# Kernel tuning notes

Hardware: AMD Instinct MI355X
Metric: run time of the kernel (lower is better)

## Reference

```python
import jax, jax.numpy as jnp
import numpy as np

N_QUBITS = 14
W_MUL = (2.0 ** 0.5) * (5.0 ** -0.5)  # he_std = gain * 5**-0.5, lrmul = 1
TWO_PI = 2.0 * np.pi


def _rx(t):
    c = jnp.cos(t / 2); s = jnp.sin(t / 2)
    return jnp.stack([jnp.stack([c + 0j, -1j * s]), jnp.stack([-1j * s, c + 0j])])


def _ry(t):
    c = jnp.cos(t / 2); s = jnp.sin(t / 2)
    return jnp.stack([jnp.stack([c + 0j, -s + 0j]), jnp.stack([s + 0j, c + 0j])])


def _rz(t):
    e = jnp.exp(-0.5j * t); z = jnp.zeros_like(e)
    return jnp.stack([jnp.stack([e, z]), jnp.stack([z, jnp.conj(e)])])


def _apply_1q(state, gate, q):
    # state: (B,) + (2,)*n ; apply 2x2 gate on qubit q (axis q+1)
    ax = q + 1
    out = jnp.tensordot(gate, state, axes=([1], [ax]))  # new qubit axis at front
    return jnp.moveaxis(out, 0, ax)


_CNOT = jnp.array([[1, 0, 0, 0],
                   [0, 1, 0, 0],
                   [0, 0, 0, 1],
                   [0, 0, 1, 0]], dtype=jnp.complex64).reshape(2, 2, 2, 2)


def _apply_cnot(state, c, t):
    # _CNOT indices: [out_c, out_t, in_c, in_t]
    out = jnp.tensordot(_CNOT, state, axes=([2, 3], [c + 1, t + 1]))
    return jnp.moveaxis(out, (0, 1), (c + 1, t + 1))


def _rot_layer(state, params, gates):
    # per-qubit triple of rotations: params[3*i + j] for gate j on qubit i
    for i in range(N_QUBITS):
        for j, g in enumerate(gates):
            state = _apply_1q(state, g(params[3 * i + j]), i)
    return state


def _ring_of_cnot(state):
    for i in range(N_QUBITS):
        state = _apply_cnot(state, i, (i + 1) % N_QUBITS)
    return state


def _forward(x_real, x_imag, weight):
    n = N_QUBITS
    B = x_real.shape[0]
    psi = (x_real + 1j * x_imag).astype(jnp.complex64).reshape((B,) + (2,) * n)
    w = weight * W_MUL
    layers = [(_rx, _ry, _rz),  # XYZLayer
              (_ry, _rz, _ry),  # YZYLayer
              (_rz, _ry, _rx),  # ZYXLayer
              (_rx, _rz, _rx),  # XZXLayer
              (_ry, _rz, _ry)]  # YZYLayer
    for li, gates in enumerate(layers):
        psi = _rot_layer(psi, w[3 * n * li: 3 * n * (li + 1)], gates)
        if li < len(layers) - 1:
            psi = _ring_of_cnot(psi)
    Z = jnp.array([[1, 0], [0, -1]], dtype=jnp.complex64)
    zpsi = _apply_1q(psi, Z, 0)
    # <psi| Z_0 |psi> (original: conj(psi) row-vector @ (Z_0 psi) column-vector, take real)
    ev = jnp.sum(jnp.conj(psi) * zpsi, axis=tuple(range(1, n + 1))).real
    return ev.reshape(B, 1)  # matches torch (B,1,1).squeeze(-1)


def setup_inputs() -> dict:
    key = jax.random.key(0)
    k1, k2, k3 = jax.random.split(key, 3)
    B = 512
    dim = 2 ** N_QUBITS
    x_real = jax.random.normal(k1, (B, 1, dim), dtype=jnp.float32)
    x_imag = jax.random.normal(k2, (B, 1, dim), dtype=jnp.float32)
    weight = jax.random.uniform(k3, (15 * N_QUBITS,), dtype=jnp.float32) * TWO_PI
    return {"x_real": x_real, "x_imag": x_imag, "weight": weight}


def reference(x_real, x_imag, weight):
    return _forward(x_real, x_imag, weight)
```

## Files before the change

### kernel.cpp

```cpp
#include <hip/hip_runtime.h>
#include <hip/hip_bf16.h>

#define NQ   14
#define DIM  16384
#define BLK  1024
#define WMUL 0.6324555320336759f

typedef float v2f __attribute__((ext_vector_type(2)));

struct C2 { float x, y; };
__device__ inline C2 cmulc(C2 a, C2 b){ return C2{a.x*b.x - a.y*b.y, a.x*b.y + a.y*b.x}; }
__device__ inline C2 caddc(C2 a, C2 b){ return C2{a.x+b.x, a.y+b.y}; }
__device__ inline void mm2(const C2* a, const C2* b, C2* o) {
    o[0] = caddc(cmulc(a[0],b[0]), cmulc(a[1],b[2]));
    o[1] = caddc(cmulc(a[0],b[1]), cmulc(a[1],b[3]));
    o[2] = caddc(cmulc(a[2],b[0]), cmulc(a[3],b[2]));
    o[3] = caddc(cmulc(a[2],b[1]), cmulc(a[3],b[3]));
}
__device__ inline void build_gate(int ty, float t, C2* g) {
    float sn, cs;
    __sincosf(0.5f * t, &sn, &cs);
    if (ty == 0) {
        g[0] = C2{cs, 0.f}; g[1] = C2{0.f, -sn};
        g[2] = C2{0.f, -sn}; g[3] = C2{cs, 0.f};
    } else if (ty == 1) {
        g[0] = C2{cs, 0.f}; g[1] = C2{-sn, 0.f};
        g[2] = C2{sn, 0.f}; g[3] = C2{cs, 0.f};
    } else {
        g[0] = C2{cs, -sn}; g[1] = C2{0.f, 0.f};
        g[2] = C2{0.f, 0.f}; g[3] = C2{cs, sn};
    }
}
__device__ const int TYPES[5][3] = {
    {0,1,2},
    {1,2,1},
    {2,1,0},
    {0,2,0},
    {1,2,1},
};

__device__ inline constexpr uint32_t slotf(uint32_t i){
    return i ^ (((i>>4) ^ (i>>8) ^ (i>>12)) & 15u);
}
template<int B> __device__ inline uint32_t ins0(uint32_t t){
    return ((t & ~((1u<<B)-1u)) << 1) | (t & ((1u<<B)-1u));
}
template<int B0,int B1,int B2> __device__ inline uint32_t expand3(uint32_t t){
    return ins0<B2>(ins0<B1>(ins0<B0>(t)));
}
template<int B0,int B1,int B2> __device__ inline constexpr uint32_t rmask3(int r){
    return ((r&1)?(1u<<B0):0u) | ((r&2)?(1u<<B1):0u) | ((r&4)?(1u<<B2):0u);
}

template<int J>
__device__ inline void rot8(v2f* v, const v2f* __restrict__ g){
    const v2f a00=g[0], b00=g[1], a01=g[2], b01=g[3];
    const v2f a10=g[4], b10=g[5], a11=g[6], b11=g[7];
    #pragma unroll
    for (int r = 0; r < 8; ++r){
        if (!(r & (1 << J))) {
            v2f x0 = v[r], x1 = v[r | (1 << J)];
            v2f s0 = x0.yx, s1 = x1.yx;
            v2f y0 = a00*x0 + b00*s0 + a01*x1 + b01*s1;
            v2f y1 = a10*x0 + b10*s0 + a11*x1 + b11*s1;
            v[r] = y0; v[r | (1<<J)] = y1;
        }
    }
}
template<int C, int T>
__device__ inline void cnot8(v2f* v){
    #pragma unroll
    for (int r = 0; r < 8; ++r){
        if ((r & (1 << C)) && !(r & (1 << T))) {
            v2f tt = v[r]; v[r] = v[r | (1 << T)]; v[r | (1 << T)] = tt;
        }
    }
}

__global__ __launch_bounds__(BLK) void qsim_kernel(
        const float* __restrict__ xr, const float* __restrict__ xi,
        const float* __restrict__ w, float* __restrict__ out) {
    __shared__ v2f s[DIM];
    __shared__ v2f gmp[5 * NQ * 8];
    __shared__ float red[BLK / 64];

    const int b   = blockIdx.x;
    const uint32_t tid = threadIdx.x;

    if (tid < 5 * NQ) {
        const int li = tid / NQ, q = tid % NQ;
        C2 M[4], G[4], T[4];
        #pragma unroll
        for (int j = 0; j < 3; ++j) {
            float t = w[3 * NQ * li + 3 * q + j] * WMUL;
            build_gate(TYPES[li][j], t, G);
            if (j == 0) { M[0]=G[0]; M[1]=G[1]; M[2]=G[2]; M[3]=G[3]; }
            else { mm2(G, M, T); M[0]=T[0]; M[1]=T[1]; M[2]=T[2]; M[3]=T[3]; }
        }
        #pragma unroll
        for (int k = 0; k < 4; ++k) {
            gmp[tid * 8 + k * 2 + 0] = v2f{ M[k].x, M[k].x};
            gmp[tid * 8 + k * 2 + 1] = v2f{-M[k].y, M[k].y};
        }
    }
    __syncthreads();

    const float* xrb = xr + (size_t)b * DIM;
    const float* xib = xi + (size_t)b * DIM;

    #define GMP(li, q) (&gmp[((li) * NQ + (q)) * 8])

    #define PASS(B0, B1, B2, ...)                                                  \
        _Pragma("unroll 1")                                                        \
        for (uint32_t sl = 0; sl < 2; ++sl) {                                      \
            const uint32_t t  = tid + sl * BLK;                                    \
            const uint32_t sb = slotf(expand3<B0,B1,B2>(t));                       \
            v2f v[8];                                                              \
            _Pragma("unroll")                                                      \
            for (int r = 0; r < 8; ++r)                                            \
                v[r] = s[sb ^ slotf(rmask3<B0,B1,B2>(r))];                         \
            __VA_ARGS__                                                            \
            _Pragma("unroll")                                                      \
            for (int r = 0; r < 8; ++r)                                            \
                s[sb ^ slotf(rmask3<B0,B1,B2>(r))] = v[r];                         \
        }                                                                          \
        __syncthreads();

    #pragma unroll 1
    for (int li = 0; li < 3; ++li) {
        #pragma unroll 1
        for (uint32_t sl = 0; sl < 2; ++sl) {
            const uint32_t t = tid + sl * BLK;
            v2f v[8];
            if (li == 0) {
                #pragma unroll
                for (int r = 0; r < 8; ++r) {
                    uint32_t i = t | ((uint32_t)r << 11);
                    v[r] = v2f{xrb[i], xib[i]};
                }
            } else {
                const uint32_t sb = slotf(expand3<11,12,13>(t));
                #pragma unroll
                for (int r = 0; r < 8; ++r)
                    v[r] = s[sb ^ slotf(rmask3<11,12,13>(r))];
            }
            rot8<2>(v, GMP(li,0)); rot8<1>(v, GMP(li,1)); rot8<0>(v, GMP(li,2));
            cnot8<2,1>(v); cnot8<1,0>(v);
            const uint32_t sb = slotf(expand3<11,12,13>(t));
            #pragma unroll
            for (int r = 0; r < 8; ++r)
                s[sb ^ slotf(rmask3<11,12,13>(r))] = v[r];
        }
        __syncthreads();

        PASS(9,10,11, rot8<1>(v, GMP(li,3));  rot8<0>(v, GMP(li,4));  cnot8<2,1>(v); cnot8<1,0>(v);)
        PASS(7,8,9,   rot8<1>(v, GMP(li,5));  rot8<0>(v, GMP(li,6));  cnot8<2,1>(v); cnot8<1,0>(v);)
        PASS(5,6,7,   rot8<1>(v, GMP(li,7));  rot8<0>(v, GMP(li,8));  cnot8<2,1>(v); cnot8<1,0>(v);)
        PASS(3,4,5,   rot8<1>(v, GMP(li,9));  rot8<0>(v, GMP(li,10)); cnot8<2,1>(v); cnot8<1,0>(v);)
        PASS(1,2,3,   rot8<1>(v, GMP(li,11)); rot8<0>(v, GMP(li,12)); cnot8<2,1>(v); cnot8<1,0>(v);)
        PASS(0,1,13,  rot8<0>(v, GMP(li,13)); cnot8<1,0>(v); cnot8<0,2>(v);)
    }

    PASS(11,12,13, rot8<2>(v, GMP(3,0));  rot8<1>(v, GMP(3,1));  rot8<0>(v, GMP(3,2));
                   cnot8<2,1>(v); cnot8<1,0>(v);
                   rot8<1>(v, GMP(4,1));)
    PASS(9,10,11,  rot8<1>(v, GMP(3,3));  rot8<0>(v, GMP(3,4));
                   cnot8<2,1>(v); cnot8<1,0>(v);
                   rot8<2>(v, GMP(4,2));  rot8<1>(v, GMP(4,3));)
    PASS(7,8,9,    rot8<1>(v, GMP(3,5));  rot8<0>(v, GMP(3,6));
                   cnot8<2,1>(v); cnot8<1,0>(v);
                   rot8<2>(v, GMP(4,4));  rot8<1>(v, GMP(4,5));)
    PASS(5,6,7,    rot8<1>(v, GMP(3,7));  rot8<0>(v, GMP(3,8));
                   cnot8<2,1>(v); cnot8<1,0>(v);
                   rot8<2>(v, GMP(4,6));  rot8<1>(v, GMP(4,7));)
    PASS(3,4,5,    rot8<1>(v, GMP(3,9));  rot8<0>(v, GMP(3,10));
                   cnot8<2,1>(v); cnot8<1,0>(v);
                   rot8<2>(v, GMP(4,8));  rot8<1>(v, GMP(4,9));)
    PASS(1,2,3,    rot8<1>(v, GMP(3,11)); rot8<0>(v, GMP(3,12));
                   cnot8<2,1>(v); cnot8<1,0>(v);
                   rot8<2>(v, GMP(4,10)); rot8<1>(v, GMP(4,11));)

    float local = 0.f;
    #pragma unroll 1
    for (uint32_t sl = 0; sl < 2; ++sl) {
        const uint32_t t  = tid + sl * BLK;
        const uint32_t sb = slotf(expand3<0,1,13>(t));
        v2f v[8];
        #pragma unroll
        for (int r = 0; r < 8; ++r)
            v[r] = s[sb ^ slotf(rmask3<0,1,13>(r))];
        rot8<0>(v, GMP(3,13));
        cnot8<1,0>(v); cnot8<0,2>(v);
        rot8<1>(v, GMP(4,12)); rot8<0>(v, GMP(4,13)); rot8<2>(v, GMP(4,0));
        #pragma unroll
        for (int r = 0; r < 8; ++r) {
            v2f p = v[r] * v[r];
            float m = p.x + p.y;
            local += (r & 4) ? -m : m;
        }
    }

    #pragma unroll
    for (int off = 32; off > 0; off >>= 1) local += __shfl_down(local, off);
    const int lane = tid & 63, wid = tid >> 6;
    if (lane == 0) red[wid] = local;
    __syncthreads();
    if (tid == 0) {
        float t = 0.f;
        #pragma unroll
        for (int k = 0; k < BLK / 64; ++k) t += red[k];
        out[b] = t;
    }
}

extern "C" void kernel_launch(void* const* d_in, const int* in_sizes, int n_in,
                              void* d_out, int out_size, void* d_ws, size_t ws_size,
                              hipStream_t stream) {
    const float* xr = (const float*)d_in[0];
    const float* xi = (const float*)d_in[1];
    const float* w  = (const float*)d_in[2];
    float* out = (float*)d_out;
    const int B = out_size;
    qsim_kernel<<<B, BLK, 0, stream>>>(xr, xi, w, out);
}
```

Baseline: 130.0 us.

## Process four qubits per shared-memory pass with 16 amplitudes per thread

Each thread now holds 16 amplitudes (4 qubit axes) in registers instead of 8 over two slots. Each pass therefore covers three new qubits, which cuts the number of shared-memory sweeps and __syncthreads barriers per layer. The cost is higher register pressure at a 1024-thread block, which could cause spills or lower occupancy.

Result: slower. 180.9 us (+39.2%).

```diff
diff --git a/kernel.cpp b/kernel.cpp
--- a/kernel.cpp
+++ b/kernel.cpp
@@ -45,19 +45,20 @@
 template<int B> __device__ inline uint32_t ins0(uint32_t t){
     return ((t & ~((1u<<B)-1u)) << 1) | (t & ((1u<<B)-1u));
 }
-template<int B0,int B1,int B2> __device__ inline uint32_t expand3(uint32_t t){
-    return ins0<B2>(ins0<B1>(ins0<B0>(t)));
-}
-template<int B0,int B1,int B2> __device__ inline constexpr uint32_t rmask3(int r){
-    return ((r&1)?(1u<<B0):0u) | ((r&2)?(1u<<B1):0u) | ((r&4)?(1u<<B2):0u);
+template<int B0,int B1,int B2,int B3> __device__ inline uint32_t expand4(uint32_t t){
+    return ins0<B3>(ins0<B2>(ins0<B1>(ins0<B0>(t))));
+}
+template<int B0,int B1,int B2,int B3> __device__ inline constexpr uint32_t rmask4(int r){
+    return ((r&1)?(1u<<B0):0u) | ((r&2)?(1u<<B1):0u)
+         | ((r&4)?(1u<<B2):0u) | ((r&8)?(1u<<B3):0u);
 }
 
 template<int J>
-__device__ inline void rot8(v2f* v, const v2f* __restrict__ g){
+__device__ inline void rot16(v2f* v, const v2f* __restrict__ g){
     const v2f a00=g[0], b00=g[1], a01=g[2], b01=g[3];
     const v2f a10=g[4], b10=g[5], a11=g[6], b11=g[7];
     #pragma unroll
-    for (int r = 0; r < 8; ++r){
+    for (int r = 0; r < 16; ++r){
         if (!(r & (1 << J))) {
             v2f x0 = v[r], x1 = v[r | (1 << J)];
             v2f s0 = x0.yx, s1 = x1.yx;
@@ -68,9 +69,9 @@
     }
 }
 template<int C, int T>
-__device__ inline void cnot8(v2f* v){
+__device__ inline void cnot16(v2f* v){
     #pragma unroll
-    for (int r = 0; r < 8; ++r){
+    for (int r = 0; r < 16; ++r){
         if ((r & (1 << C)) && !(r & (1 << T))) {
             v2f tt = v[r]; v[r] = v[r | (1 << T)]; v[r | (1 << T)] = tt;
         }
@@ -110,93 +111,84 @@
 
     #define GMP(li, q) (&gmp[((li) * NQ + (q)) * 8])
 
-    #define PASS(B0, B1, B2, ...)                                                  \
-        _Pragma("unroll 1")                                                        \
-        for (uint32_t sl = 0; sl < 2; ++sl) {                                      \
-            const uint32_t t  = tid + sl * BLK;                                    \
-            const uint32_t sb = slotf(expand3<B0,B1,B2>(t));                       \
-            v2f v[8];                                                              \
+    #define PASS(B0, B1, B2, B3, ...)                                              \
+        {                                                                          \
+            const uint32_t sb = slotf(expand4<B0,B1,B2,B3>(tid));                  \
+            v2f v[16];                                                             \
             _Pragma("unroll")                                                      \
-            for (int r = 0; r < 8; ++r)                                            \
-                v[r] = s[sb ^ slotf(rmask3<B0,B1,B2>(r))];                         \
+            for (int r = 0; r < 16; ++r)                                           \
+                v[r] = s[sb ^ slotf(rmask4<B0,B1,B2,B3>(r))];                      \
             __VA_ARGS__                                                            \
             _Pragma("unroll")                                                      \
-            for (int r = 0; r < 8; ++r)                                            \
-                s[sb ^ slotf(rmask3<B0,B1,B2>(r))] = v[r];                         \
+            for (int r = 0; r < 16; ++r)                                           \
+                s[sb ^ slotf(rmask4<B0,B1,B2,B3>(r))] = v[r];                      \
         }                                                                          \
         __syncthreads();
 
     #pragma unroll 1
     for (int li = 0; li < 3; ++li) {
-        #pragma unroll 1
-        for (uint32_t sl = 0; sl < 2; ++sl) {
-            const uint32_t t = tid + sl * BLK;
-            v2f v[8];
+        {
+            v2f v[16];
             if (li == 0) {
                 #pragma unroll
-                for (int r = 0; r < 8; ++r) {
-                    uint32_t i = t | ((uint32_t)r << 11);
+                for (int r = 0; r < 16; ++r) {
+                    uint32_t i = tid | ((uint32_t)r << 10);
                     v[r] = v2f{xrb[i], xib[i]};
                 }
             } else {
-                const uint32_t sb = slotf(expand3<11,12,13>(t));
+                const uint32_t sb = slotf(expand4<10,11,12,13>(tid));
                 #pragma unroll
-                for (int r = 0; r < 8; ++r)
-                    v[r] = s[sb ^ slotf(rmask3<11,12,13>(r))];
+                for (int r = 0; r < 16; ++r)
+                    v[r] = s[sb ^ slotf(rmask4<10,11,12,13>(r))];
             }
-            rot8<2>(v, GMP(li,0)); rot8<1>(v, GMP(li,1)); rot8<0>(v, GMP(li,2));
-            cnot8<2,1>(v); cnot8<1,0>(v);
-            const uint32_t sb = slotf(expand3<11,12,13>(t));
+            rot16<3>(v, GMP(li,0)); rot16<2>(v, GMP(li,1));
+            rot16<1>(v, GMP(li,2)); rot16<0>(v, GMP(li,3));
+            cnot16<3,2>(v); cnot16<2,1>(v); cnot16<1,0>(v);
+            const uint32_t sb = slotf(expand4<10,11,12,13>(tid));
             #pragma unroll
-            for (int r = 0; r < 8; ++r)
-                s[sb ^ slotf(rmask3<11,12,13>(r))] = v[r];
+            for (int r = 0; r < 16; ++r)
+                s[sb ^ slotf(rmask4<10,11,12,13>(r))] = v[r];
         }
         __syncthreads();
 
-        PASS(9,10,11, rot8<1>(v, GMP(li,3));  rot8<0>(v, GMP(li,4));  cnot8<2,1>(v); cnot8<1,0>(v);)
-        PASS(7,8,9,   rot8<1>(v, GMP(li,5));  rot8<0>(v, GMP(li,6));  cnot8<2,1>(v); cnot8<1,0>(v);)
-        PASS(5,6,7,   rot8<1>(v, GMP(li,7));  rot8<0>(v, GMP(li,8));  cnot8<2,1>(v); cnot8<1,0>(v);)
-        PASS(3,4,5,   rot8<1>(v, GMP(li,9));  rot8<0>(v, GMP(li,10)); cnot8<2,1>(v); cnot8<1,0>(v);)
-        PASS(1,2,3,   rot8<1>(v, GMP(li,11)); rot8<0>(v, GMP(li,12)); cnot8<2,1>(v); cnot8<1,0>(v);)
-        PASS(0,1,13,  rot8<0>(v, GMP(li,13)); cnot8<1,0>(v); cnot8<0,2>(v);)
-    }
-
-    PASS(11,12,13, rot8<2>(v, GMP(3,0));  rot8<1>(v, GMP(3,1));  rot8<0>(v, GMP(3,2));
-                   cnot8<2,1>(v); cnot8<1,0>(v);
-                   rot8<1>(v, GMP(4,1));)
-    PASS(9,10,11,  rot8<1>(v, GMP(3,3));  rot8<0>(v, GMP(3,4));
-                   cnot8<2,1>(v); cnot8<1,0>(v);
-                   rot8<2>(v, GMP(4,2));  rot8<1>(v, GMP(4,3));)
-    PASS(7,8,9,    rot8<1>(v, GMP(3,5));  rot8<0>(v, GMP(3,6));
-                   cnot8<2,1>(v); cnot8<1,0>(v);
-                   rot8<2>(v, GMP(4,4));  rot8<1>(v, GMP(4,5));)
-    PASS(5,6,7,    rot8<1>(v, GMP(3,7));  rot8<0>(v, GMP(3,8));
-                   cnot8<2,1>(v); cnot8<1,0>(v);
-                   rot8<2>(v, GMP(4,6));  rot8<1>(v, GMP(4,7));)
-    PASS(3,4,5,    rot8<1>(v, GMP(3,9));  rot8<0>(v, GMP(3,10));
-                   cnot8<2,1>(v); cnot8<1,0>(v);
-                   rot8<2>(v, GMP(4,8));  rot8<1>(v, GMP(4,9));)
-    PASS(1,2,3,    rot8<1>(v, GMP(3,11)); rot8<0>(v, GMP(3,12));
-                   cnot8<2,1>(v); cnot8<1,0>(v);
-                   rot8<2>(v, GMP(4,10)); rot8<1>(v, GMP(4,11));)
+        PASS(7,8,9,10, rot16<2>(v, GMP(li,4)); rot16<1>(v, GMP(li,5)); rot16<0>(v, GMP(li,6));
+                       cnot16<3,2>(v); cnot16<2,1>(v); cnot16<1,0>(v);)
+        PASS(4,5,6,7,  rot16<2>(v, GMP(li,7)); rot16<1>(v, GMP(li,8)); rot16<0>(v, GMP(li,9));
+                       cnot16<3,2>(v); cnot16<2,1>(v); cnot16<1,0>(v);)
+        PASS(1,2,3,4,  rot16<2>(v, GMP(li,10)); rot16<1>(v, GMP(li,11)); rot16<0>(v, GMP(li,12));
+                       cnot16<3,2>(v); cnot16<2,1>(v); cnot16<1,0>(v);)
+        PASS(0,1,2,13, rot16<0>(v, GMP(li,13)); cnot16<1,0>(v); cnot16<0,3>(v);)
+    }
+
+    PASS(10,11,12,13, rot16<3>(v, GMP(3,0));  rot16<2>(v, GMP(3,1));
+                      rot16<1>(v, GMP(3,2));  rot16<0>(v, GMP(3,3));
+                      cnot16<3,2>(v); cnot16<2,1>(v); cnot16<1,0>(v);
+                      rot16<2>(v, GMP(4,1));  rot16<1>(v, GMP(4,2));)
+    PASS(7,8,9,10,    rot16<2>(v, GMP(3,4));  rot16<1>(v, GMP(3,5));  rot16<0>(v, GMP(3,6));
+                      cnot16<3,2>(v); cnot16<2,1>(v); cnot16<1,0>(v);
+                      rot16<3>(v, GMP(4,3));  rot16<2>(v, GMP(4,4));  rot16<1>(v, GMP(4,5));)
+    PASS(4,5,6,7,     rot16<2>(v, GMP(3,7));  rot16<1>(v, GMP(3,8));  rot16<0>(v, GMP(3,9));
+                      cnot16<3,2>(v); cnot16<2,1>(v); cnot16<1,0>(v);
+                      rot16<3>(v, GMP(4,6));  rot16<2>(v, GMP(4,7));  rot16<1>(v, GMP(4,8));)
+    PASS(1,2,3,4,     rot16<2>(v, GMP(3,10)); rot16<1>(v, GMP(3,11)); rot16<0>(v, GMP(3,12));
+                      cnot16<3,2>(v); cnot16<2,1>(v); cnot16<1,0>(v);
+                      rot16<3>(v, GMP(4,9));  rot16<2>(v, GMP(4,10)); rot16<1>(v, GMP(4,11));)
 
     float local = 0.f;
-    #pragma unroll 1
-    for (uint32_t sl = 0; sl < 2; ++sl) {
-        const uint32_t t  = tid + sl * BLK;
-        const uint32_t sb = slotf(expand3<0,1,13>(t));
-        v2f v[8];
-        #pragma unroll
-        for (int r = 0; r < 8; ++r)
-            v[r] = s[sb ^ slotf(rmask3<0,1,13>(r))];
-        rot8<0>(v, GMP(3,13));
-        cnot8<1,0>(v); cnot8<0,2>(v);
-        rot8<1>(v, GMP(4,12)); rot8<0>(v, GMP(4,13)); rot8<2>(v, GMP(4,0));
-        #pragma unroll
-        for (int r = 0; r < 8; ++r) {
+    {
+        const uint32_t sb = slotf(expand4<0,1,2,13>(tid));
+        v2f v[16];
+        #pragma unroll
+        for (int r = 0; r < 16; ++r)
+            v[r] = s[sb ^ slotf(rmask4<0,1,2,13>(r))];
+        rot16<0>(v, GMP(3,13));
+        cnot16<1,0>(v); cnot16<0,3>(v);
+        rot16<1>(v, GMP(4,12)); rot16<0>(v, GMP(4,13)); rot16<3>(v, GMP(4,0));
+        #pragma unroll
+        for (int r = 0; r < 16; ++r) {
             v2f p = v[r] * v[r];
             float m = p.x + p.y;
-            local += (r & 4) ? -m : m;
+            local += (r & 8) ? -m : m;
         }
     }
 
```

## Map qubits onto wavefront lanes and use cross-lane swizzles to cut shared-memory passes

Applied to the files above, without the earlier changes.

Restructures the state-vector simulation so each thread holds 3 qubits in registers while 6 more qubits map onto wavefront lane bits. Rotations and CNOTs on lane qubits use ds_swizzle and shfl_xor exchanges. This cuts the number of LDS round-trip passes and barriers from about 25 to 9 and uses a new swizzle for bank-conflict avoidance. The trade-off is extra cross-lane shuffle instructions per gate and intricate qubit-to-index bookkeeping that risks correctness errors.

New measurement: 217.8 us. +67.6%, slower.

```diff
diff --git a/kernel.cpp b/kernel.cpp
--- a/kernel.cpp
+++ b/kernel.cpp
@@ -1,5 +1,4 @@
 #include <hip/hip_runtime.h>
-#include <hip/hip_bf16.h>
 
 #define NQ   14
 #define DIM  16384
@@ -39,21 +38,24 @@
     {1,2,1},
 };
 
-__device__ inline constexpr uint32_t slotf(uint32_t i){
-    return i ^ (((i>>4) ^ (i>>8) ^ (i>>12)) & 15u);
-}
-template<int B> __device__ inline uint32_t ins0(uint32_t t){
-    return ((t & ~((1u<<B)-1u)) << 1) | (t & ((1u<<B)-1u));
-}
-template<int B0,int B1,int B2> __device__ inline uint32_t expand3(uint32_t t){
-    return ins0<B2>(ins0<B1>(ins0<B0>(t)));
-}
-template<int B0,int B1,int B2> __device__ inline constexpr uint32_t rmask3(int r){
-    return ((r&1)?(1u<<B0):0u) | ((r&2)?(1u<<B1):0u) | ((r&4)?(1u<<B2):0u);
+__device__ __forceinline__ constexpr uint32_t slotf2(uint32_t i){
+    return i ^ ((((i>>4) ^ (i>>8) ^ ((i>>12)<<2)) & 15u));
+}
+
+template<int M>
+__device__ __forceinline__ v2f shflx(v2f x){
+    if constexpr (M < 32) {
+        constexpr int pat = 0x1F | (M << 10);
+        int a = __builtin_amdgcn_ds_swizzle(__float_as_int(x.x), pat);
+        int b = __builtin_amdgcn_ds_swizzle(__float_as_int(x.y), pat);
+        return v2f{__int_as_float(a), __int_as_float(b)};
+    } else {
+        return v2f{__shfl_xor(x.x, 32, 64), __shfl_xor(x.y, 32, 64)};
+    }
 }
 
 template<int J>
-__device__ inline void rot8(v2f* v, const v2f* __restrict__ g){
+__device__ __forceinline__ void rot8(v2f* v, const v2f* __restrict__ g){
     const v2f a00=g[0], b00=g[1], a01=g[2], b01=g[3];
     const v2f a10=g[4], b10=g[5], a11=g[6], b11=g[7];
     #pragma unroll
@@ -67,15 +69,46 @@
         }
     }
 }
+
+template<int LM>
+__device__ __forceinline__ void rotL(v2f* v, const v2f* __restrict__ g, uint32_t lane){
+    const bool hi = (lane & LM) != 0;
+    const v2f c1 = hi ? g[6] : g[0];
+    const v2f c2 = hi ? g[7] : g[1];
+    const v2f c3 = hi ? g[4] : g[2];
+    const v2f c4 = hi ? g[5] : g[3];
+    #pragma unroll
+    for (int r = 0; r < 8; ++r){
+        v2f x  = v[r];
+        v2f xp = shflx<LM>(x);
+        v[r] = c1*x + c2*x.yx + c3*xp + c4*xp.yx;
+    }
+}
+
 template<int C, int T>
-__device__ inline void cnot8(v2f* v){
+__device__ __forceinline__ void cnotRR(v2f* v){
+    #pragma unroll
+    for (int r = 0; r < 8; ++r)
+        if ((r & (1<<C)) && !(r & (1<<T))) {
+            v2f t = v[r]; v[r] = v[r|(1<<T)]; v[r|(1<<T)] = t;
+        }
+}
+template<int C, int TM>
+__device__ __forceinline__ void cnotRL(v2f* v){
+    #pragma unroll
+    for (int r = 0; r < 8; ++r)
+        if (r & (1<<C)) v[r] = shflx<TM>(v[r]);
+}
+template<int CM, int TM>
+__device__ __forceinline__ void cnotLL(v2f* v, uint32_t lane){
+    const bool c = (lane & CM) != 0;
     #pragma unroll
     for (int r = 0; r < 8; ++r){
-        if ((r & (1 << C)) && !(r & (1 << T))) {
-            v2f tt = v[r]; v[r] = v[r | (1 << T)]; v[r | (1 << T)] = tt;
-        }
-    }
-}
+        v2f p = shflx<TM>(v[r]);
+        v[r] = c ? p : v[r];
+    }
+}
+
 
 __global__ __launch_bounds__(BLK) void qsim_kernel(
         const float* __restrict__ xr, const float* __restrict__ xi,
@@ -85,7 +118,8 @@
     __shared__ float red[BLK / 64];
 
     const int b   = blockIdx.x;
-    const uint32_t tid = threadIdx.x;
+    const uint32_t tid  = threadIdx.x;
+    const uint32_t lane = tid & 63u;
 
     if (tid < 5 * NQ) {
         const int li = tid / NQ, q = tid % NQ;
@@ -110,100 +144,107 @@
 
     #define GMP(li, q) (&gmp[((li) * NQ + (q)) * 8])
 
-    #define PASS(B0, B1, B2, ...)                                                  \
-        _Pragma("unroll 1")                                                        \
-        for (uint32_t sl = 0; sl < 2; ++sl) {                                      \
-            const uint32_t t  = tid + sl * BLK;                                    \
-            const uint32_t sb = slotf(expand3<B0,B1,B2>(t));                       \
-            v2f v[8];                                                              \
-            _Pragma("unroll")                                                      \
-            for (int r = 0; r < 8; ++r)                                            \
-                v[r] = s[sb ^ slotf(rmask3<B0,B1,B2>(r))];                         \
-            __VA_ARGS__                                                            \
-            _Pragma("unroll")                                                      \
-            for (int r = 0; r < 8; ++r)                                            \
-                s[sb ^ slotf(rmask3<B0,B1,B2>(r))] = v[r];                         \
-        }                                                                          \
+    #pragma unroll 1
+    for (uint32_t sl = 0; sl < 2; ++sl) {
+        const uint32_t t = tid + sl * BLK;
+        v2f v[8];
+        #pragma unroll
+        for (int r = 0; r < 8; ++r) {
+            uint32_t i = t | ((uint32_t)r << 11);
+            v[r] = v2f{xrb[i], xib[i]};
+        }
+        rot8<2>(v, GMP(0,0)); rot8<1>(v, GMP(0,1)); rot8<0>(v, GMP(0,2));
+        rotL<1 >(v, GMP(0,13), lane); rotL<2 >(v, GMP(0,12), lane);
+        rotL<4 >(v, GMP(0,11), lane); rotL<8 >(v, GMP(0,10), lane);
+        rotL<16>(v, GMP(0,9),  lane); rotL<32>(v, GMP(0,8),  lane);
+        cnotRR<2,1>(v);
+        cnotRR<1,0>(v);
+        const uint32_t sb = slotf2(t);
+        #pragma unroll
+        for (int r = 0; r < 8; ++r) s[sb ^ slotf2((uint32_t)r << 11)] = v[r];
+    }
+    __syncthreads();
+
+    #define PASS_M(...)                                                         \
+        _Pragma("unroll 1")                                                     \
+        for (uint32_t sl = 0; sl < 2; ++sl) {                                   \
+            const uint32_t base = (lane << 3) | ((tid >> 6) & 7u)               \
+                                | (((tid >> 9) & 1u) << 12) | (sl << 13);       \
+            const uint32_t sb = slotf2(base);                                   \
+            v2f v[8];                                                           \
+            _Pragma("unroll")                                                   \
+            for (int r = 0; r < 8; ++r) v[r] = s[sb ^ slotf2((uint32_t)r<<9)];  \
+            __VA_ARGS__                                                         \
+            _Pragma("unroll")                                                   \
+            for (int r = 0; r < 8; ++r) s[sb ^ slotf2((uint32_t)r<<9)] = v[r];  \
+        }                                                                       \
         __syncthreads();
 
-    #pragma unroll 1
-    for (int li = 0; li < 3; ++li) {
-        #pragma unroll 1
-        for (uint32_t sl = 0; sl < 2; ++sl) {
-            const uint32_t t = tid + sl * BLK;
-            v2f v[8];
-            if (li == 0) {
-                #pragma unroll
-                for (int r = 0; r < 8; ++r) {
-                    uint32_t i = t | ((uint32_t)r << 11);
-                    v[r] = v2f{xrb[i], xib[i]};
-                }
-            } else {
-                const uint32_t sb = slotf(expand3<11,12,13>(t));
-                #pragma unroll
-                for (int r = 0; r < 8; ++r)
-                    v[r] = s[sb ^ slotf(rmask3<11,12,13>(r))];
-            }
-            rot8<2>(v, GMP(li,0)); rot8<1>(v, GMP(li,1)); rot8<0>(v, GMP(li,2));
-            cnot8<2,1>(v); cnot8<1,0>(v);
-            const uint32_t sb = slotf(expand3<11,12,13>(t));
-            #pragma unroll
-            for (int r = 0; r < 8; ++r)
-                s[sb ^ slotf(rmask3<11,12,13>(r))] = v[r];
-        }
+    #define PASS_B(...)                                                         \
+        _Pragma("unroll 1")                                                     \
+        for (uint32_t sl = 0; sl < 2; ++sl) {                                   \
+            const uint32_t base = (lane & 3u) | (((lane >> 2) & 1u) << 5)       \
+                                | (((lane >> 3) & 7u) << 11)                    \
+                                | (((tid >> 6) & 15u) << 6) | (sl << 10);       \
+            const uint32_t sb = slotf2(base);                                   \
+            v2f v[8];                                                           \
+            _Pragma("unroll")                                                   \
+            for (int r = 0; r < 8; ++r) v[r] = s[sb ^ slotf2((uint32_t)r<<2)];  \
+            __VA_ARGS__                                                         \
+            _Pragma("unroll")                                                   \
+            for (int r = 0; r < 8; ++r) s[sb ^ slotf2((uint32_t)r<<2)] = v[r];  \
+        }                                                                       \
         __syncthreads();
 
-        PASS(9,10,11, rot8<1>(v, GMP(li,3));  rot8<0>(v, GMP(li,4));  cnot8<2,1>(v); cnot8<1,0>(v);)
-        PASS(7,8,9,   rot8<1>(v, GMP(li,5));  rot8<0>(v, GMP(li,6));  cnot8<2,1>(v); cnot8<1,0>(v);)
-        PASS(5,6,7,   rot8<1>(v, GMP(li,7));  rot8<0>(v, GMP(li,8));  cnot8<2,1>(v); cnot8<1,0>(v);)
-        PASS(3,4,5,   rot8<1>(v, GMP(li,9));  rot8<0>(v, GMP(li,10)); cnot8<2,1>(v); cnot8<1,0>(v);)
-        PASS(1,2,3,   rot8<1>(v, GMP(li,11)); rot8<0>(v, GMP(li,12)); cnot8<2,1>(v); cnot8<1,0>(v);)
-        PASS(0,1,13,  rot8<0>(v, GMP(li,13)); cnot8<1,0>(v); cnot8<0,2>(v);)
-    }
-
-    PASS(11,12,13, rot8<2>(v, GMP(3,0));  rot8<1>(v, GMP(3,1));  rot8<0>(v, GMP(3,2));
-                   cnot8<2,1>(v); cnot8<1,0>(v);
-                   rot8<1>(v, GMP(4,1));)
-    PASS(9,10,11,  rot8<1>(v, GMP(3,3));  rot8<0>(v, GMP(3,4));
-                   cnot8<2,1>(v); cnot8<1,0>(v);
-                   rot8<2>(v, GMP(4,2));  rot8<1>(v, GMP(4,3));)
-    PASS(7,8,9,    rot8<1>(v, GMP(3,5));  rot8<0>(v, GMP(3,6));
-                   cnot8<2,1>(v); cnot8<1,0>(v);
-                   rot8<2>(v, GMP(4,4));  rot8<1>(v, GMP(4,5));)
-    PASS(5,6,7,    rot8<1>(v, GMP(3,7));  rot8<0>(v, GMP(3,8));
-                   cnot8<2,1>(v); cnot8<1,0>(v);
-                   rot8<2>(v, GMP(4,6));  rot8<1>(v, GMP(4,7));)
-    PASS(3,4,5,    rot8<1>(v, GMP(3,9));  rot8<0>(v, GMP(3,10));
-                   cnot8<2,1>(v); cnot8<1,0>(v);
-                   rot8<2>(v, GMP(4,8));  rot8<1>(v, GMP(4,9));)
-    PASS(1,2,3,    rot8<1>(v, GMP(3,11)); rot8<0>(v, GMP(3,12));
-                   cnot8<2,1>(v); cnot8<1,0>(v);
-                   rot8<2>(v, GMP(4,10)); rot8<1>(v, GMP(4,11));)
+    #define MID(li)                                                             \
+        rot8<1>(v, GMP(li,3)); rot8<0>(v, GMP(li,4));                           \
+        rotL<32>(v, GMP(li,5), lane); rotL<16>(v, GMP(li,6), lane);             \
+        rotL<8 >(v, GMP(li,7), lane);                                           \
+        cnotRR<2,1>(v); cnotRR<1,0>(v); cnotRL<0,32>(v);                        \
+        cnotLL<32,16>(v, lane); cnotLL<16,8>(v, lane);                          \
+        cnotLL<8,4>(v, lane); cnotLL<4,2>(v, lane);
+
+    #define TAILROT(n)                                                          \
+        cnotRR<2,1>(v); cnotRR<1,0>(v); cnotRL<0,2>(v);                         \
+        cnotLL<2,1>(v, lane); cnotLL<1,32>(v, lane);                            \
+        rot8<2>(v, GMP(n,9)); rot8<1>(v, GMP(n,10)); rot8<0>(v, GMP(n,11));     \
+        rotL<2 >(v, GMP(n,12), lane); rotL<1 >(v, GMP(n,13), lane);             \
+        rotL<32>(v, GMP(n,0),  lane); rotL<16>(v, GMP(n,1),  lane);             \
+        rotL<8 >(v, GMP(n,2),  lane); rotL<4 >(v, GMP(n,8),  lane);
+
+    #define HEAD cnotLL<32,16>(v, lane); cnotLL<16,8>(v, lane);
+
+    PASS_M(MID(0))
+    PASS_B(TAILROT(1) HEAD)
+    PASS_M(MID(1))
+    PASS_B(TAILROT(2) HEAD)
+    PASS_M(MID(2))
+    PASS_B(TAILROT(3) HEAD)
+    PASS_M(MID(3))
+    PASS_B(TAILROT(4))
 
     float local = 0.f;
     #pragma unroll 1
     for (uint32_t sl = 0; sl < 2; ++sl) {
-        const uint32_t t  = tid + sl * BLK;
-        const uint32_t sb = slotf(expand3<0,1,13>(t));
+        const uint32_t base = (lane << 3) | ((tid >> 6) & 7u)
+                            | (((tid >> 9) & 1u) << 12) | (sl << 13);
+        const uint32_t sb = slotf2(base);
         v2f v[8];
         #pragma unroll
-        for (int r = 0; r < 8; ++r)
-            v[r] = s[sb ^ slotf(rmask3<0,1,13>(r))];
-        rot8<0>(v, GMP(3,13));
-        cnot8<1,0>(v); cnot8<0,2>(v);
-        rot8<1>(v, GMP(4,12)); rot8<0>(v, GMP(4,13)); rot8<2>(v, GMP(4,0));
-        #pragma unroll
-        for (int r = 0; r < 8; ++r) {
-            v2f p = v[r] * v[r];
-            float m = p.x + p.y;
-            local += (r & 4) ? -m : m;
-        }
+        for (int r = 0; r < 8; ++r) v[r] = s[sb ^ slotf2((uint32_t)r << 9)];
+        rot8<1>(v, GMP(4,3)); rot8<0>(v, GMP(4,4));
+        rotL<32>(v, GMP(4,5), lane); rotL<16>(v, GMP(4,6), lane);
+        rotL<8 >(v, GMP(4,7), lane);
+        float acc = 0.f;
+        #pragma unroll
+        for (int r = 0; r < 8; ++r) { v2f p = v[r] * v[r]; acc += p.x + p.y; }
+        local += sl ? -acc : acc;
     }
 
     #pragma unroll
     for (int off = 32; off > 0; off >>= 1) local += __shfl_down(local, off);
-    const int lane = tid & 63, wid = tid >> 6;
-    if (lane == 0) red[wid] = local;
+    const int wid = tid >> 6;
+    if ((tid & 63u) == 0) red[wid] = local;
     __syncthreads();
     if (tid == 0) {
         float t = 0.f;
```

## Apply low-qubit gates via cross-lane DPP/swizzle shuffles to cut shared-memory passes

Applied to the files above, without the earlier changes.

Low qubits (0-5) now map to lane bits of the wavefront, so their rotations and CNOTs are done with DPP, ds_swizzle and bpermute register exchanges instead of separate shared-memory passes. Each layer now needs three LDS passes plus the load pass instead of six, and the last two layers share the same loop structure. This cuts LDS traffic and block barriers. In exchange it adds cross-lane instructions, a bpermute-based CNOT chain across lane bits, and sched barriers, which raises register and instruction pressure and makes correctness depend on exact lane mapping.

Result: slower. 144.4 us (+11.1%).

```diff
diff --git a/kernel.cpp b/kernel.cpp
--- a/kernel.cpp
+++ b/kernel.cpp
@@ -1,5 +1,4 @@
 #include <hip/hip_runtime.h>
-#include <hip/hip_bf16.h>
 
 #define NQ   14
 #define DIM  16384
@@ -52,30 +51,88 @@
     return ((r&1)?(1u<<B0):0u) | ((r&2)?(1u<<B1):0u) | ((r&4)?(1u<<B2):0u);
 }
 
+#define SBAR __builtin_amdgcn_sched_barrier(0)
+
+template<int M>
+__device__ __forceinline__ v2f shflx(v2f x){
+    int a = __float_as_int(x.x), b = __float_as_int(x.y);
+    int ra, rb;
+    if constexpr (M == 1) {
+        ra = __builtin_amdgcn_mov_dpp(a, 0xB1, 0xF, 0xF, false);
+        rb = __builtin_amdgcn_mov_dpp(b, 0xB1, 0xF, 0xF, false);
+    } else if constexpr (M == 2) {
+        ra = __builtin_amdgcn_mov_dpp(a, 0x4E, 0xF, 0xF, false);
+        rb = __builtin_amdgcn_mov_dpp(b, 0x4E, 0xF, 0xF, false);
+    } else if constexpr (M == 8) {
+        ra = __builtin_amdgcn_mov_dpp(a, 0x128, 0xF, 0xF, false);
+        rb = __builtin_amdgcn_mov_dpp(b, 0x128, 0xF, 0xF, false);
+    } else if constexpr (M < 32) {
+        constexpr int pat = 0x1F | (M << 10);
+        ra = __builtin_amdgcn_ds_swizzle(a, pat);
+        rb = __builtin_amdgcn_ds_swizzle(b, pat);
+    } else {
+        ra = __shfl_xor(a, 32, 64);
+        rb = __shfl_xor(b, 32, 64);
+    }
+    return v2f{__int_as_float(ra), __int_as_float(rb)};
+}
+
+
 template<int J>
-__device__ inline void rot8(v2f* v, const v2f* __restrict__ g){
+__device__ __forceinline__ void rot8(v2f* v, const v2f* __restrict__ g){
     const v2f a00=g[0], b00=g[1], a01=g[2], b01=g[3];
-    const v2f a10=g[4], b10=g[5], a11=g[6], b11=g[7];
+    const v2f a11=g[4], b11=g[5], a10=g[6], b10=g[7];
     #pragma unroll
     for (int r = 0; r < 8; ++r){
         if (!(r & (1 << J))) {
             v2f x0 = v[r], x1 = v[r | (1 << J)];
             v2f s0 = x0.yx, s1 = x1.yx;
-            v2f y0 = a00*x0 + b00*s0 + a01*x1 + b01*s1;
-            v2f y1 = a10*x0 + b10*s0 + a11*x1 + b11*s1;
-            v[r] = y0; v[r | (1<<J)] = y1;
-        }
+            v[r]          = a00*x0 + b00*s0 + a01*x1 + b01*s1;
+            v[r | (1<<J)] = a10*x0 + b10*s0 + a11*x1 + b11*s1;
+        }
+    }
+}
+template<int LM>
+__device__ __forceinline__ void rotL(v2f* v, const v2f* __restrict__ g, uint32_t lane){
+    const v2f* gl = g + ((lane & LM) ? 4 : 0);
+    const v2f c1 = gl[0], c2 = gl[1], c3 = gl[2], c4 = gl[3];
+    #pragma unroll
+    for (int r = 0; r < 8; ++r){
+        v2f x  = v[r];
+        v2f xp = shflx<LM>(x);
+        v[r] = c1*x + c2*x.yx + c3*xp + c4*xp.yx;
     }
 }
 template<int C, int T>
-__device__ inline void cnot8(v2f* v){
-    #pragma unroll
-    for (int r = 0; r < 8; ++r){
-        if ((r & (1 << C)) && !(r & (1 << T))) {
-            v2f tt = v[r]; v[r] = v[r | (1 << T)]; v[r | (1 << T)] = tt;
-        }
-    }
-}
+__device__ __forceinline__ void cnotRR(v2f* v){
+    #pragma unroll
+    for (int r = 0; r < 8; ++r)
+        if ((r & (1<<C)) && !(r & (1<<T))) {
+            v2f t = v[r]; v[r] = v[r|(1<<T)]; v[r|(1<<T)] = t;
+        }
+}
+template<int C, int M>
+__device__ __forceinline__ void cnotRL(v2f* v){
+    #pragma unroll
+    for (int r = 0; r < 8; ++r)
+        if (r & (1<<C)) v[r] = shflx<M>(v[r]);
+}
+template<int CM, int T>
+__device__ __forceinline__ void cnotLR(v2f* v, uint32_t lane){
+    const bool c = (lane & CM) != 0;
+    #pragma unroll
+    for (int r = 0; r < 8; ++r)
+        if (!(r & (1 << T))) {
+            v2f lo = v[r], hi = v[r | (1 << T)];
+            v[r]          = c ? hi : lo;
+            v[r | (1<<T)] = c ? lo : hi;
+        }
+}
+__device__ __forceinline__ v2f bperm1(v2f x, int addr){
+    return v2f{__int_as_float(__builtin_amdgcn_ds_bpermute(addr, __float_as_int(x.x))),
+               __int_as_float(__builtin_amdgcn_ds_bpermute(addr, __float_as_int(x.y)))};
+}
+
 
 __global__ __launch_bounds__(BLK) void qsim_kernel(
         const float* __restrict__ xr, const float* __restrict__ xi,
@@ -84,8 +141,10 @@
     __shared__ v2f gmp[5 * NQ * 8];
     __shared__ float red[BLK / 64];
 
-    const int b   = blockIdx.x;
-    const uint32_t tid = threadIdx.x;
+    const int b    = blockIdx.x;
+    const uint32_t tid  = threadIdx.x;
+    const uint32_t lane = tid & 63u;
+    const int csrc = (int)((lane ^ ((lane >> 1) & 15u)) << 2);
 
     if (tid < 5 * NQ) {
         const int li = tid / NQ, q = tid % NQ;
@@ -97,11 +156,11 @@
             if (j == 0) { M[0]=G[0]; M[1]=G[1]; M[2]=G[2]; M[3]=G[3]; }
             else { mm2(G, M, T); M[0]=T[0]; M[1]=T[1]; M[2]=T[2]; M[3]=T[3]; }
         }
-        #pragma unroll
-        for (int k = 0; k < 4; ++k) {
-            gmp[tid * 8 + k * 2 + 0] = v2f{ M[k].x, M[k].x};
-            gmp[tid * 8 + k * 2 + 1] = v2f{-M[k].y, M[k].y};
-        }
+        v2f* gb = &gmp[tid * 8];
+        gb[0] = v2f{ M[0].x, M[0].x}; gb[1] = v2f{-M[0].y, M[0].y};
+        gb[2] = v2f{ M[1].x, M[1].x}; gb[3] = v2f{-M[1].y, M[1].y};
+        gb[4] = v2f{ M[3].x, M[3].x}; gb[5] = v2f{-M[3].y, M[3].y};
+        gb[6] = v2f{ M[2].x, M[2].x}; gb[7] = v2f{-M[2].y, M[2].y};
     }
     __syncthreads();
 
@@ -126,8 +185,10 @@
         }                                                                          \
         __syncthreads();
 
+    #define CHAIN { _Pragma("unroll") for (int r = 0; r < 8; ++r) v[r] = bperm1(v[r], csrc); }
+
     #pragma unroll 1
-    for (int li = 0; li < 3; ++li) {
+    for (int li = 0; li < 4; ++li) {
         #pragma unroll 1
         for (uint32_t sl = 0; sl < 2; ++sl) {
             const uint32_t t = tid + sl * BLK;
@@ -143,9 +204,11 @@
                 #pragma unroll
                 for (int r = 0; r < 8; ++r)
                     v[r] = s[sb ^ slotf(rmask3<11,12,13>(r))];
+                cnotLR<1,2>(v, lane);
             }
-            rot8<2>(v, GMP(li,0)); rot8<1>(v, GMP(li,1)); rot8<0>(v, GMP(li,2));
-            cnot8<2,1>(v); cnot8<1,0>(v);
+            rot8<2>(v, GMP(li,0)); rot8<1>(v, GMP(li,1)); SBAR;
+            rot8<0>(v, GMP(li,2));
+            cnotRR<2,1>(v); cnotRR<1,0>(v);
             const uint32_t sb = slotf(expand3<11,12,13>(t));
             #pragma unroll
             for (int r = 0; r < 8; ++r)
@@ -153,45 +216,47 @@
         }
         __syncthreads();
 
-        PASS(9,10,11, rot8<1>(v, GMP(li,3));  rot8<0>(v, GMP(li,4));  cnot8<2,1>(v); cnot8<1,0>(v);)
-        PASS(7,8,9,   rot8<1>(v, GMP(li,5));  rot8<0>(v, GMP(li,6));  cnot8<2,1>(v); cnot8<1,0>(v);)
-        PASS(5,6,7,   rot8<1>(v, GMP(li,7));  rot8<0>(v, GMP(li,8));  cnot8<2,1>(v); cnot8<1,0>(v);)
-        PASS(3,4,5,   rot8<1>(v, GMP(li,9));  rot8<0>(v, GMP(li,10)); cnot8<2,1>(v); cnot8<1,0>(v);)
-        PASS(1,2,3,   rot8<1>(v, GMP(li,11)); rot8<0>(v, GMP(li,12)); cnot8<2,1>(v); cnot8<1,0>(v);)
-        PASS(0,1,13,  rot8<0>(v, GMP(li,13)); cnot8<1,0>(v); cnot8<0,2>(v);)
-    }
-
-    PASS(11,12,13, rot8<2>(v, GMP(3,0));  rot8<1>(v, GMP(3,1));  rot8<0>(v, GMP(3,2));
-                   cnot8<2,1>(v); cnot8<1,0>(v);
-                   rot8<1>(v, GMP(4,1));)
-    PASS(9,10,11,  rot8<1>(v, GMP(3,3));  rot8<0>(v, GMP(3,4));
-                   cnot8<2,1>(v); cnot8<1,0>(v);
-                   rot8<2>(v, GMP(4,2));  rot8<1>(v, GMP(4,3));)
-    PASS(7,8,9,    rot8<1>(v, GMP(3,5));  rot8<0>(v, GMP(3,6));
-                   cnot8<2,1>(v); cnot8<1,0>(v);
-                   rot8<2>(v, GMP(4,4));  rot8<1>(v, GMP(4,5));)
-    PASS(5,6,7,    rot8<1>(v, GMP(3,7));  rot8<0>(v, GMP(3,8));
-                   cnot8<2,1>(v); cnot8<1,0>(v);
-                   rot8<2>(v, GMP(4,6));  rot8<1>(v, GMP(4,7));)
-    PASS(3,4,5,    rot8<1>(v, GMP(3,9));  rot8<0>(v, GMP(3,10));
-                   cnot8<2,1>(v); cnot8<1,0>(v);
-                   rot8<2>(v, GMP(4,8));  rot8<1>(v, GMP(4,9));)
-    PASS(1,2,3,    rot8<1>(v, GMP(3,11)); rot8<0>(v, GMP(3,12));
-                   cnot8<2,1>(v); cnot8<1,0>(v);
-                   rot8<2>(v, GMP(4,10)); rot8<1>(v, GMP(4,11));)
+        PASS(9,10,11,
+            rot8<1>(v, GMP(li,3)); rot8<0>(v, GMP(li,4)); SBAR;
+            rotL<1>(v, GMP(li,13), lane); rotL<2>(v, GMP(li,12), lane); SBAR;
+            rotL<4>(v, GMP(li,11), lane);
+            cnotRR<2,1>(v); cnotRR<1,0>(v);
+            if (li == 3) { SBAR; rot8<1>(v, GMP(4,3)); }
+        )
+        PASS(7,8,9,
+            rot8<1>(v, GMP(li,5)); rot8<0>(v, GMP(li,6)); SBAR;
+            rotL<8>(v, GMP(li,10), lane); rotL<16>(v, GMP(li,9), lane); SBAR;
+            rotL<32>(v, GMP(li,8), lane);
+            cnotRR<2,1>(v); cnotRR<1,0>(v);
+            if (li == 3) { SBAR; rot8<2>(v, GMP(4,4)); rot8<1>(v, GMP(4,5)); }
+        )
+        PASS(5,6,7,
+            rot8<1>(v, GMP(li,7));
+            cnotRR<2,1>(v); cnotRR<1,0>(v);
+            cnotRL<0,16>(v);
+            CHAIN
+            if (li == 3) {
+                SBAR; rot8<2>(v, GMP(4,6)); rot8<1>(v, GMP(4,7)); SBAR;
+                rot8<0>(v, GMP(4,8)); rotL<16>(v, GMP(4,9), lane); SBAR;
+                rotL<8>(v, GMP(4,10), lane); rotL<4>(v, GMP(4,11), lane); SBAR;
+                rotL<2>(v, GMP(4,12), lane);
+            }
+        )
+    }
 
     float local = 0.f;
     #pragma unroll 1
     for (uint32_t sl = 0; sl < 2; ++sl) {
         const uint32_t t  = tid + sl * BLK;
-        const uint32_t sb = slotf(expand3<0,1,13>(t));
+        const uint32_t sb = slotf(expand3<11,12,13>(t));
         v2f v[8];
         #pragma unroll
         for (int r = 0; r < 8; ++r)
-            v[r] = s[sb ^ slotf(rmask3<0,1,13>(r))];
-        rot8<0>(v, GMP(3,13));
-        cnot8<1,0>(v); cnot8<0,2>(v);
-        rot8<1>(v, GMP(4,12)); rot8<0>(v, GMP(4,13)); rot8<2>(v, GMP(4,0));
+            v[r] = s[sb ^ slotf(rmask3<11,12,13>(r))];
+        cnotLR<1,2>(v, lane);
+        rotL<1>(v, GMP(4,13), lane); SBAR;
+        rot8<2>(v, GMP(4,0)); rot8<1>(v, GMP(4,1)); SBAR;
+        rot8<0>(v, GMP(4,2));
         #pragma unroll
         for (int r = 0; r < 8; ++r) {
             v2f p = v[r] * v[r];
@@ -202,8 +267,8 @@
 
     #pragma unroll
     for (int off = 32; off > 0; off >>= 1) local += __shfl_down(local, off);
-    const int lane = tid & 63, wid = tid >> 6;
-    if (lane == 0) red[wid] = local;
+    const int wid = tid >> 6;
+    if ((tid & 63u) == 0) red[wid] = local;
     __syncthreads();
     if (tid == 0) {
         float t = 0.f;
```
